# Kernel optimization log

Measured on AMD Instinct MI355X. Metric: run time of the kernel, lower is better.

## Reference

```python
import jax, jax.numpy as jnp
import numpy as np

VIEWS, N, D = 6, 20000, 512
BN_EPS = 1e-5


def setup_inputs() -> dict:
    key = jax.random.key(0)
    ks = jax.random.split(key, 8)
    s = 1.0 / np.sqrt(D)
    u = lambda k, shape: jax.random.uniform(k, shape, jnp.float32, -s, s)
    return {
        "latent_feature": jax.random.normal(ks[0], (VIEWS, N, D), jnp.float32),
        "WQ_w": u(ks[1], (D, D)), "WQ_b": u(ks[2], (D,)),
        "WK_w": u(ks[3], (D, D)), "WK_b": u(ks[4], (D,)),
        "WV_w": u(ks[5], (D, D)), "WV_b": u(ks[6], (D,)),
        "g_q": jnp.ones((D,), jnp.float32), "b_q": jnp.zeros((D,), jnp.float32),
        "g_k": jnp.ones((D,), jnp.float32), "b_k": jnp.zeros((D,), jnp.float32),
        "g_v": jnp.ones((D,), jnp.float32), "b_v": jnp.zeros((D,), jnp.float32),
    }


def _batchnorm(x, gamma, beta):
    # BatchNorm1d in training mode: stats over all (view, N) samples per channel
    mean = jnp.mean(x, axis=(0, 1), keepdims=True)
    var = jnp.mean((x - mean) ** 2, axis=(0, 1), keepdims=True)  # biased var
    return gamma * (x - mean) * jax.lax.rsqrt(var + BN_EPS) + beta


def _fro_normalize(x):
    # Frobenius norm per view over (N, D)
    n = jnp.sqrt(jnp.sum(x * x, axis=(1, 2), keepdims=True)) + 1e-8
    return x / n


def _multi_projection(P):
    dim = P.shape[0]
    P = 0.5 * (jax.nn.softmax(P, axis=0) + jax.nn.softmax(P, axis=1))
    for _ in range(10):  # fixed 10-step doubly-stochastic projection
        P1 = jnp.maximum(P, 0.0)
        P2 = P1 - (jnp.sum(P1, axis=1, keepdims=True) - 1.0) / dim
        P = P2 - (jnp.sum(P2, axis=0, keepdims=True) - 1.0) / dim
    return P


def reference(latent_feature, WQ_w, WQ_b, WK_w, WK_b, WV_w, WV_b,
              g_q, b_q, g_k, b_k, g_v, b_v):
    # latent_feature: [views, N, D]
    Q = _batchnorm(latent_feature @ WQ_w.T + WQ_b, g_q, b_q)
    K = _batchnorm(latent_feature @ WK_w.T + WK_b, g_k, b_k)
    V = _batchnorm(latent_feature @ WV_w.T + WV_b, g_v, b_v)
    Q, K, V = _fro_normalize(Q), _fro_normalize(K), _fro_normalize(V)
    P = jax.nn.sigmoid(jnp.einsum('ind,jnd->ij', Q, K))  # [views, views]
    P = _multi_projection(P)
    return jnp.einsum('ij,ind->jnd', P, V)  # [views, N, D]
```

## Files before the change

### kernel.cpp

```cpp
#include <hip/hip_runtime.h>

#define VIEWS 6
#define NPTS 20000
#define DIM 512
#define M_TOTAL (VIEWS * NPTS)

typedef __bf16 bf16_t;
typedef __attribute__((ext_vector_type(8))) __bf16 bf16x8;
typedef __attribute__((ext_vector_type(4))) float f32x4;

#define OFF_XB 0L
#define OFF_QB 122880000L
#define OFF_KB 245760000L
#define OFF_VB 368640000L
#define OFF_WB 491520000L
#define OFF_F32 493092864L
#define S_SUM 0
#define S_SSQ 9216
#define S_PPRE 18432
#define S_COEFA 18468
#define S_COEFC 20004
#define S_INVN 21540
#define S_P 21558
#define S_END 21594

__device__ __forceinline__ void gload_lds16(const void* gsrc, void* lds) {
    __builtin_amdgcn_global_load_lds(
        (const __attribute__((address_space(1))) unsigned int*)gsrc,
        (__attribute__((address_space(3))) unsigned int*)lds,
        16, 0, 0);
}

__global__ __launch_bounds__(256) void convert_bf16(
    const float* __restrict__ src, bf16_t* __restrict__ dst, long n8)
{
    long i = (long)blockIdx.x * blockDim.x + threadIdx.x;
    const long stride = (long)gridDim.x * blockDim.x;
    for (; i < n8; i += stride) {
        const float4* s = (const float4*)(src + i * 8);
        float4 x = s[0], y = s[1];
        bf16x8 o;
        o[0] = (bf16_t)x.x; o[1] = (bf16_t)x.y; o[2] = (bf16_t)x.z; o[3] = (bf16_t)x.w;
        o[4] = (bf16_t)y.x; o[5] = (bf16_t)y.y; o[6] = (bf16_t)y.z; o[7] = (bf16_t)y.w;
        *(bf16x8*)(dst + i * 8) = o;
    }
}

__global__ __launch_bounds__(256) void gemm_qkv_mfma(
    const bf16_t* __restrict__ XB, const bf16_t* __restrict__ WB,
    const float* __restrict__ b0, const float* __restrict__ b1,
    const float* __restrict__ b2,
    float* __restrict__ statS, float* __restrict__ statQ,
    bf16_t* __restrict__ QB, bf16_t* __restrict__ KB, bf16_t* __restrict__ VB)
{
    const int v  = blockIdx.z;
    const int n0 = blockIdx.x * 128;
    const int ct = blockIdx.y;
    const int t  = ct >> 2;
    const int c0 = (ct & 3) * 128;

    const int tid  = threadIdx.x;
    const int wid  = tid >> 6;
    const int lane = tid & 63;
    const int lr   = lane & 15;
    const int lk   = lane >> 4;
    const int wm   = wid >> 1;
    const int wn   = wid & 1;
    const int nvalid = min(128, NPTS - n0);

    __shared__ unsigned short As[128][64];
    __shared__ unsigned short Bs[128][64];
    __shared__ float redS[128];
    __shared__ float redQ[128];

    const bf16_t* Ag = XB + ((long)v * NPTS + n0) * DIM;
    const bf16_t* Bg = WB + ((long)t << 18) + ((long)c0 << 9);
    bf16_t* Obuf = (t == 0) ? QB : (t == 1) ? KB : VB;
    const float* bias = (t == 0) ? b0 : (t == 1) ? b1 : b2;

    f32x4 acc[4][4];
    const f32x4 zero4 = {0.f, 0.f, 0.f, 0.f};
#pragma unroll
    for (int i = 0; i < 4; ++i)
#pragma unroll
        for (int j = 0; j < 4; ++j) acc[i][j] = zero4;

    for (int k0 = 0; k0 < DIM; k0 += 64) {
        __syncthreads();
#pragma unroll
        for (int i = 0; i < 4; ++i) {
            const int base = i * 256 + wid * 64;
            const int myf  = base + lane;
            const int row  = myf >> 3;
            const int kc   = myf & 7;
            const int rowc = (row < nvalid) ? row : (nvalid - 1);
            gload_lds16(Ag + (long)rowc * DIM + k0 + kc * 8,
                        ((char*)&As[0][0]) + (long)base * 16);
            gload_lds16(Bg + (long)row * DIM + k0 + kc * 8,
                        ((char*)&Bs[0][0]) + (long)base * 16);
        }
        __syncthreads();
#pragma unroll
        for (int ks = 0; ks < 2; ++ks) {
            bf16x8 af[4], bfr[4];
#pragma unroll
            for (int f = 0; f < 4; ++f) {
                af[f]  = *(const bf16x8*)&As[wm * 64 + f * 16 + lr][ks * 32 + lk * 8];
                bfr[f] = *(const bf16x8*)&Bs[wn * 64 + f * 16 + lr][ks * 32 + lk * 8];
            }
#pragma unroll
            for (int fm = 0; fm < 4; ++fm)
#pragma unroll
                for (int fn = 0; fn < 4; ++fn)
                    acc[fm][fn] = __builtin_amdgcn_mfma_f32_16x16x32_bf16(
                        af[fm], bfr[fn], acc[fm][fn], 0, 0, 0);
        }
    }

    __syncthreads();
    if (tid < 128) { redS[tid] = 0.f; redQ[tid] = 0.f; }
    __syncthreads();

    float bcol[4];
#pragma unroll
    for (int fn = 0; fn < 4; ++fn) bcol[fn] = bias[c0 + wn * 64 + fn * 16 + lr];

#pragma unroll
    for (int fn = 0; fn < 4; ++fn) {
        float cs = 0.f, cq = 0.f;
        const int col = c0 + wn * 64 + fn * 16 + lr;
#pragma unroll
        for (int fm = 0; fm < 4; ++fm) {
            const int rbase = wm * 64 + fm * 16 + lk * 4;
#pragma unroll
            for (int r = 0; r < 4; ++r) {
                const int row = rbase + r;
                if (row < nvalid) {
                    float val = acc[fm][fn][r] + bcol[fn];
                    cs += val;
                    cq += val * val;
                    Obuf[((long)v * NPTS + n0 + row) * DIM + col] = (bf16_t)val;
                }
            }
        }
        atomicAdd(&redS[wn * 64 + fn * 16 + lr], cs);
        atomicAdd(&redQ[wn * 64 + fn * 16 + lr], cq);
    }
    __syncthreads();
    if (tid < 128) {
        atomicAdd(&statS[(((long)t * 6 + v) << 9) + c0 + tid], redS[tid]);
        atomicAdd(&statQ[(((long)t * 6 + v) << 9) + c0 + tid], redQ[tid]);
    }
}

__global__ __launch_bounds__(512) void finalize_stats(
    const float* __restrict__ gq, const float* __restrict__ beq,
    const float* __restrict__ gk, const float* __restrict__ bek,
    const float* __restrict__ gv, const float* __restrict__ bev,
    float* __restrict__ ws2)
{
    const int t = blockIdx.x;
    const int c = threadIdx.x;
    const float* g  = (t == 0) ? gq : (t == 1) ? gk : gv;
    const float* be = (t == 0) ? beq : (t == 1) ? bek : bev;
    const float* sumbuf = ws2 + S_SUM + (long)t * 6 * 512;
    const float* ssqbuf = ws2 + S_SSQ + (long)t * 6 * 512;

    float s[6], q[6];
    float tot = 0.f, totq = 0.f;
#pragma unroll
    for (int v = 0; v < 6; ++v) {
        s[v] = sumbuf[v * 512 + c];
        q[v] = ssqbuf[v * 512 + c];
        tot += s[v]; totq += q[v];
    }
    const float invM = 1.0f / (float)M_TOTAL;
    float mean = tot * invM;
    float var  = totq * invM - mean * mean;
    float a    = g[c] * rsqrtf(var + 1e-5f);
    float cc   = be[c] - a * mean;
    ws2[S_COEFA + t * 512 + c] = a;
    ws2[S_COEFC + t * 512 + c] = cc;

    __shared__ float red[512];
    for (int v = 0; v < 6; ++v) {
        red[c] = a * a * q[v] + 2.f * a * cc * s[v] + (float)NPTS * cc * cc;
        __syncthreads();
        for (int off = 256; off > 0; off >>= 1) {
            if (c < off) red[c] += red[c + off];
            __syncthreads();
        }
        if (c == 0) ws2[S_INVN + t * 6 + v] = 1.f / (sqrtf(red[0]) + 1e-8f);
        __syncthreads();
    }
}

__global__ __launch_bounds__(256) void qk_dot(
    const bf16_t* __restrict__ QB, const bf16_t* __restrict__ KB,
    float* __restrict__ ws2)
{
    float acc[36];
#pragma unroll
    for (int c = 0; c < 36; ++c) acc[c] = 0.f;

    const float* cA = ws2 + S_COEFA;
    const long total = (long)NPTS * 64;
    for (long it = (long)blockIdx.x * 256 + threadIdx.x; it < total;
         it += (long)gridDim.x * 256) {
        const int n  = (int)(it >> 6);
        const int d8 = (int)(it & 63);

        float w8[8];
#pragma unroll
        for (int e = 0; e < 8; ++e)
            w8[e] = cA[d8 * 8 + e] * cA[512 + d8 * 8 + e];

        float qw[6][8];
#pragma unroll
        for (int i = 0; i < 6; ++i) {
            bf16x8 qv = *(const bf16x8*)(QB + ((long)i * NPTS + n) * DIM + d8 * 8);
#pragma unroll
            for (int e = 0; e < 8; ++e) qw[i][e] = (float)qv[e] * w8[e];
        }
#pragma unroll
        for (int j = 0; j < 6; ++j) {
            bf16x8 kv = *(const bf16x8*)(KB + ((long)j * NPTS + n) * DIM + d8 * 8);
            float kf[8];
#pragma unroll
            for (int e = 0; e < 8; ++e) kf[e] = (float)kv[e];
#pragma unroll
            for (int i = 0; i < 6; ++i) {
                float d = 0.f;
#pragma unroll
                for (int e = 0; e < 8; ++e) d = fmaf(qw[i][e], kf[e], d);
                acc[i * 6 + j] += d;
            }
        }
    }

    __shared__ float part[36];
    if (threadIdx.x < 36) part[threadIdx.x] = 0.f;
    __syncthreads();
    const int lane = threadIdx.x & 63;
#pragma unroll
    for (int c = 0; c < 36; ++c) {
        float x = acc[c];
#pragma unroll
        for (int m = 1; m < 64; m <<= 1) x += __shfl_xor(x, m);
        if (lane == 0) atomicAdd(&part[c], x);
    }
    __syncthreads();
    if (threadIdx.x < 36) atomicAdd(&ws2[S_PPRE + threadIdx.x], part[threadIdx.x]);
}

__global__ __launch_bounds__(512) void project_kernel(float* __restrict__ ws2)
{
    const int c = threadIdx.x;
    __shared__ float red[512];
    const float aq = ws2[S_COEFA + c],       cq = ws2[S_COEFC + c];
    const float ak = ws2[S_COEFA + 512 + c], ck = ws2[S_COEFC + 512 + c];

    float vals[13];
#pragma unroll
    for (int i = 0; i < 6; ++i) vals[i]     = aq * ck * ws2[S_SUM + i * 512 + c];
#pragma unroll
    for (int j = 0; j < 6; ++j) vals[6 + j] = cq * ak * ws2[S_SUM + (6 + j) * 512 + c];
    vals[12] = cq * ck;

    float out13[13];
#pragma unroll
    for (int r = 0; r < 13; ++r) {
        red[c] = vals[r];
        __syncthreads();
        for (int off = 256; off > 0; off >>= 1) {
            if (c < off) red[c] += red[c + off];
            __syncthreads();
        }
        out13[r] = red[0];
        __syncthreads();
    }

    if (c != 0) return;

    const float* invn = ws2 + S_INVN;
    float p[6][6];
    for (int i = 0; i < 6; ++i)
        for (int j = 0; j < 6; ++j) {
            float raw = ws2[S_PPRE + i * 6 + j] + out13[i] + out13[6 + j] +
                        (float)NPTS * out13[12];
            float z = raw * invn[i] * invn[6 + j];
            p[i][j] = 1.f / (1.f + expf(-z));
        }
    float s0[6][6], s1[6][6];
    for (int j = 0; j < 6; ++j) {
        float m = -1e30f;
        for (int i = 0; i < 6; ++i) m = fmaxf(m, p[i][j]);
        float sum = 0.f;
        for (int i = 0; i < 6; ++i) { s0[i][j] = expf(p[i][j] - m); sum += s0[i][j]; }
        for (int i = 0; i < 6; ++i) s0[i][j] /= sum;
    }
    for (int i = 0; i < 6; ++i) {
        float m = -1e30f;
        for (int j = 0; j < 6; ++j) m = fmaxf(m, p[i][j]);
        float sum = 0.f;
        for (int j = 0; j < 6; ++j) { s1[i][j] = expf(p[i][j] - m); sum += s1[i][j]; }
        for (int j = 0; j < 6; ++j) s1[i][j] /= sum;
    }
    for (int i = 0; i < 6; ++i)
        for (int j = 0; j < 6; ++j) p[i][j] = 0.5f * (s0[i][j] + s1[i][j]);

    for (int itr = 0; itr < 10; ++itr) {
        float p1[6][6];
        for (int i = 0; i < 6; ++i)
            for (int j = 0; j < 6; ++j) p1[i][j] = fmaxf(p[i][j], 0.f);
        for (int i = 0; i < 6; ++i) {
            float rs = 0.f;
            for (int j = 0; j < 6; ++j) rs += p1[i][j];
            float adj = (rs - 1.f) * (1.f / 6.f);
            for (int j = 0; j < 6; ++j) p1[i][j] -= adj;
        }
        for (int j = 0; j < 6; ++j) {
            float cs = 0.f;
            for (int i = 0; i < 6; ++i) cs += p1[i][j];
            float adj = (cs - 1.f) * (1.f / 6.f);
            for (int i = 0; i < 6; ++i) p1[i][j] -= adj;
        }
        for (int i = 0; i < 6; ++i)
            for (int j = 0; j < 6; ++j) p[i][j] = p1[i][j];
    }
    for (int i = 0; i < 6; ++i)
        for (int j = 0; j < 6; ++j) ws2[S_P + i * 6 + j] = p[i][j];
}

__global__ __launch_bounds__(256) void combine_out(
    const bf16_t* __restrict__ VB, const float* __restrict__ ws2,
    float* __restrict__ out)
{
    float w[36];
#pragma unroll
    for (int c = 0; c < 36; ++c)
        w[c] = ws2[S_P + c] * ws2[S_INVN + 12 + c / 6];
    const float* av = ws2 + S_COEFA + 1024;
    const float* cv = ws2 + S_COEFC + 1024;

    const long total = (long)NPTS * 64;
    for (long it = (long)blockIdx.x * 256 + threadIdx.x; it < total;
         it += (long)gridDim.x * 256) {
        const int n  = (int)(it >> 6);
        const int d8 = (int)(it & 63);
        float a8[8], c8[8];
#pragma unroll
        for (int e = 0; e < 8; ++e) { a8[e] = av[d8 * 8 + e]; c8[e] = cv[d8 * 8 + e]; }

        float o[6][8];
#pragma unroll
        for (int j = 0; j < 6; ++j)
#pragma unroll
            for (int e = 0; e < 8; ++e) o[j][e] = 0.f;

#pragma unroll
        for (int i = 0; i < 6; ++i) {
            bf16x8 xv = *(const bf16x8*)(VB + ((long)i * NPTS + n) * DIM + d8 * 8);
            float vn[8];
#pragma unroll
            for (int e = 0; e < 8; ++e) vn[e] = fmaf(a8[e], (float)xv[e], c8[e]);
#pragma unroll
            for (int j = 0; j < 6; ++j) {
                const float wi = w[i * 6 + j];
#pragma unroll
                for (int e = 0; e < 8; ++e) o[j][e] = fmaf(wi, vn[e], o[j][e]);
            }
        }
#pragma unroll
        for (int j = 0; j < 6; ++j) {
            float* dst = out + ((long)j * NPTS + n) * DIM + d8 * 8;
            *(float4*)dst       = *(const float4*)&o[j][0];
            *(float4*)(dst + 4) = *(const float4*)&o[j][4];
        }
    }
}

extern "C" void kernel_launch(void* const* d_in, const int* in_sizes, int n_in,
                              void* d_out, int out_size, void* d_ws, size_t ws_size,
                              hipStream_t stream)
{
    const float* X   = (const float*)d_in[0];
    const float* Wq  = (const float*)d_in[1];
    const float* bq  = (const float*)d_in[2];
    const float* Wk  = (const float*)d_in[3];
    const float* bk  = (const float*)d_in[4];
    const float* Wv  = (const float*)d_in[5];
    const float* bv  = (const float*)d_in[6];
    const float* gq  = (const float*)d_in[7];
    const float* beq = (const float*)d_in[8];
    const float* gk  = (const float*)d_in[9];
    const float* bek = (const float*)d_in[10];
    const float* gv  = (const float*)d_in[11];
    const float* bev = (const float*)d_in[12];

    char* w = (char*)d_ws;
    bf16_t* XB = (bf16_t*)(w + OFF_XB);
    bf16_t* QB = (bf16_t*)(w + OFF_QB);
    bf16_t* KB = (bf16_t*)(w + OFF_KB);
    bf16_t* VB = (bf16_t*)(w + OFF_VB);
    bf16_t* WB = (bf16_t*)(w + OFF_WB);
    float* ws2 = (float*)(w + OFF_F32);
    float* out = (float*)d_out;

    hipMemsetAsync(ws2, 0, S_END * sizeof(float), stream);

    convert_bf16<<<2048, 256, 0, stream>>>(X, XB, (long)M_TOTAL * DIM / 8);
    convert_bf16<<<128, 256, 0, stream>>>(Wq, WB,           (long)DIM * DIM / 8);
    convert_bf16<<<128, 256, 0, stream>>>(Wk, WB + 262144,  (long)DIM * DIM / 8);
    convert_bf16<<<128, 256, 0, stream>>>(Wv, WB + 524288,  (long)DIM * DIM / 8);

    dim3 g1(157, 12, 6);
    gemm_qkv_mfma<<<g1, 256, 0, stream>>>(XB, WB, bq, bk, bv,
                                          ws2 + S_SUM, ws2 + S_SSQ, QB, KB, VB);
    finalize_stats<<<3, 512, 0, stream>>>(gq, beq, gk, bek, gv, bev, ws2);
    qk_dot<<<2048, 256, 0, stream>>>(QB, KB, ws2);
    project_kernel<<<1, 512, 0, stream>>>(ws2);
    combine_out<<<2048, 256, 0, stream>>>(VB, ws2, out);
}
```

Baseline: 1.110 ms.

## Fuse Q/K/V tiles sharing one A tile, swizzle LDS, remap blocks for XCD locality

Each GEMM block now loads one 64-row tile of X and computes 64 columns for all three of Q, K and V, so the A tile is reused three times instead of being loaded separately per projection. LDS rows use an XOR swizzle on the 16-byte chunk index to avoid bank conflicts. A 1D grid with an XCD-aware remap (orig&7 stride) places neighbouring tiles on the same chiplet for L2 reuse, and launch bounds request 4 blocks per CU. Tiles are smaller (64x64x3), which raises the number of blocks and adds per-block epilogue syncs for the three stat reductions.

After: 1.113 ms. About the same (+0.3%).

```diff
diff --git a/kernel.cpp b/kernel.cpp
--- a/kernel.cpp
+++ b/kernel.cpp
@@ -46,18 +46,21 @@
     }
 }
 
-__global__ __launch_bounds__(256) void gemm_qkv_mfma(
+__global__ __launch_bounds__(256, 4) void gemm_qkv_mfma(
     const bf16_t* __restrict__ XB, const bf16_t* __restrict__ WB,
     const float* __restrict__ b0, const float* __restrict__ b1,
     const float* __restrict__ b2,
     float* __restrict__ statS, float* __restrict__ statQ,
     bf16_t* __restrict__ QB, bf16_t* __restrict__ KB, bf16_t* __restrict__ VB)
 {
-    const int v  = blockIdx.z;
-    const int n0 = blockIdx.x * 128;
-    const int ct = blockIdx.y;
-    const int t  = ct >> 2;
-    const int c0 = (ct & 3) * 128;
+    const int orig = blockIdx.x;
+    const int L    = (orig & 7) * 1878 + (orig >> 3);
+    const int n0i  = L / 48;
+    const int rem  = L - n0i * 48;
+    const int v    = rem >> 3;
+    const int c0   = (rem & 7) << 6;
+    const int n0   = n0i * 64;
+    const int nvalid = min(64, NPTS - n0);
 
     const int tid  = threadIdx.x;
     const int wid  = tid >> 6;
@@ -66,90 +69,104 @@
     const int lk   = lane >> 4;
     const int wm   = wid >> 1;
     const int wn   = wid & 1;
-    const int nvalid = min(128, NPTS - n0);
-
-    __shared__ unsigned short As[128][64];
-    __shared__ unsigned short Bs[128][64];
-    __shared__ float redS[128];
-    __shared__ float redQ[128];
+
+    __shared__ char smem[32768];
 
     const bf16_t* Ag = XB + ((long)v * NPTS + n0) * DIM;
-    const bf16_t* Bg = WB + ((long)t << 18) + ((long)c0 << 9);
-    bf16_t* Obuf = (t == 0) ? QB : (t == 1) ? KB : VB;
-    const float* bias = (t == 0) ? b0 : (t == 1) ? b1 : b2;
-
-    f32x4 acc[4][4];
+
+    f32x4 acc[3][2][2];
     const f32x4 zero4 = {0.f, 0.f, 0.f, 0.f};
 #pragma unroll
-    for (int i = 0; i < 4; ++i)
-#pragma unroll
-        for (int j = 0; j < 4; ++j) acc[i][j] = zero4;
+    for (int t = 0; t < 3; ++t)
+#pragma unroll
+        for (int i = 0; i < 2; ++i)
+#pragma unroll
+            for (int j = 0; j < 2; ++j) acc[t][i][j] = zero4;
 
     for (int k0 = 0; k0 < DIM; k0 += 64) {
         __syncthreads();
 #pragma unroll
-        for (int i = 0; i < 4; ++i) {
+        for (int i = 0; i < 8; ++i) {
             const int base = i * 256 + wid * 64;
-            const int myf  = base + lane;
-            const int row  = myf >> 3;
-            const int kc   = myf & 7;
-            const int rowc = (row < nvalid) ? row : (nvalid - 1);
-            gload_lds16(Ag + (long)rowc * DIM + k0 + kc * 8,
-                        ((char*)&As[0][0]) + (long)base * 16);
-            gload_lds16(Bg + (long)row * DIM + k0 + kc * 8,
-                        ((char*)&Bs[0][0]) + (long)base * 16);
+            const int g    = base + lane;
+            const bf16_t* src;
+            if (g < 512) {
+                const int row = g >> 3;
+                const int kcs = (g & 7) ^ (row & 7);
+                const int rowc = (row < nvalid) ? row : (nvalid - 1);
+                src = Ag + (long)rowc * DIM + k0 + kcs * 8;
+            } else {
+                const int h   = g - 512;
+                const int t   = h >> 9;
+                const int idx = h & 511;
+                const int row = idx >> 3;
+                const int kcs = (idx & 7) ^ (row & 7);
+                src = WB + ((long)t << 18) + (long)(c0 + row) * DIM + k0 + kcs * 8;
+            }
+            gload_lds16(src, smem + (long)base * 16);
         }
         __syncthreads();
 #pragma unroll
         for (int ks = 0; ks < 2; ++ks) {
-            bf16x8 af[4], bfr[4];
-#pragma unroll
-            for (int f = 0; f < 4; ++f) {
-                af[f]  = *(const bf16x8*)&As[wm * 64 + f * 16 + lr][ks * 32 + lk * 8];
-                bfr[f] = *(const bf16x8*)&Bs[wn * 64 + f * 16 + lr][ks * 32 + lk * 8];
-            }
-#pragma unroll
-            for (int fm = 0; fm < 4; ++fm)
-#pragma unroll
-                for (int fn = 0; fn < 4; ++fn)
-                    acc[fm][fn] = __builtin_amdgcn_mfma_f32_16x16x32_bf16(
-                        af[fm], bfr[fn], acc[fm][fn], 0, 0, 0);
+            const int kc = ks * 4 + lk;
+            bf16x8 af[2];
+#pragma unroll
+            for (int fm = 0; fm < 2; ++fm) {
+                const int rowA = wm * 32 + fm * 16 + lr;
+                af[fm] = *(const bf16x8*)(smem + rowA * 128 + ((kc ^ (rowA & 7)) << 4));
+            }
+#pragma unroll
+            for (int t = 0; t < 3; ++t) {
+#pragma unroll
+                for (int fn = 0; fn < 2; ++fn) {
+                    const int rowB = wn * 32 + fn * 16 + lr;
+                    bf16x8 bf = *(const bf16x8*)(smem + 8192 + t * 8192 +
+                                                 rowB * 128 + ((kc ^ (rowB & 7)) << 4));
+#pragma unroll
+                    for (int fm = 0; fm < 2; ++fm)
+                        acc[t][fm][fn] = __builtin_amdgcn_mfma_f32_16x16x32_bf16(
+                            af[fm], bf, acc[t][fm][fn], 0, 0, 0);
+                }
+            }
         }
     }
 
     __syncthreads();
-    if (tid < 128) { redS[tid] = 0.f; redQ[tid] = 0.f; }
-    __syncthreads();
-
-    float bcol[4];
-#pragma unroll
-    for (int fn = 0; fn < 4; ++fn) bcol[fn] = bias[c0 + wn * 64 + fn * 16 + lr];
-
-#pragma unroll
-    for (int fn = 0; fn < 4; ++fn) {
-        float cs = 0.f, cq = 0.f;
-        const int col = c0 + wn * 64 + fn * 16 + lr;
-#pragma unroll
-        for (int fm = 0; fm < 4; ++fm) {
-            const int rbase = wm * 64 + fm * 16 + lk * 4;
-#pragma unroll
-            for (int r = 0; r < 4; ++r) {
-                const int row = rbase + r;
-                if (row < nvalid) {
-                    float val = acc[fm][fn][r] + bcol[fn];
-                    cs += val;
-                    cq += val * val;
-                    Obuf[((long)v * NPTS + n0 + row) * DIM + col] = (bf16_t)val;
+    float* redS = (float*)smem;
+    float* redQ = redS + 64;
+    for (int t = 0; t < 3; ++t) {
+        if (tid < 128) redS[tid] = 0.f;
+        __syncthreads();
+        bf16_t* Obuf = (t == 0) ? QB : (t == 1) ? KB : VB;
+        const float* bias = (t == 0) ? b0 : (t == 1) ? b1 : b2;
+#pragma unroll
+        for (int fn = 0; fn < 2; ++fn) {
+            const int cl  = wn * 32 + fn * 16 + lr;
+            const int col = c0 + cl;
+            const float bv_ = bias[col];
+            float cs = 0.f, cq = 0.f;
+#pragma unroll
+            for (int fm = 0; fm < 2; ++fm) {
+#pragma unroll
+                for (int r = 0; r < 4; ++r) {
+                    const int row = wm * 32 + fm * 16 + lk * 4 + r;
+                    if (row < nvalid) {
+                        float val = acc[t][fm][fn][r] + bv_;
+                        cs += val;
+                        cq += val * val;
+                        Obuf[((long)v * NPTS + n0 + row) * DIM + col] = (bf16_t)val;
+                    }
                 }
             }
-        }
-        atomicAdd(&redS[wn * 64 + fn * 16 + lr], cs);
-        atomicAdd(&redQ[wn * 64 + fn * 16 + lr], cq);
-    }
-    __syncthreads();
-    if (tid < 128) {
-        atomicAdd(&statS[(((long)t * 6 + v) << 9) + c0 + tid], redS[tid]);
-        atomicAdd(&statQ[(((long)t * 6 + v) << 9) + c0 + tid], redQ[tid]);
+            atomicAdd(&redS[cl], cs);
+            atomicAdd(&redQ[cl], cq);
+        }
+        __syncthreads();
+        if (tid < 64) {
+            atomicAdd(&statS[(((long)t * 6 + v) << 9) + c0 + tid], redS[tid]);
+            atomicAdd(&statQ[(((long)t * 6 + v) << 9) + c0 + tid], redQ[tid]);
+        }
+        __syncthreads();
     }
 }
 
@@ -414,9 +431,8 @@
     convert_bf16<<<128, 256, 0, stream>>>(Wk, WB + 262144,  (long)DIM * DIM / 8);
     convert_bf16<<<128, 256, 0, stream>>>(Wv, WB + 524288,  (long)DIM * DIM / 8);
 
-    dim3 g1(157, 12, 6);
-    gemm_qkv_mfma<<<g1, 256, 0, stream>>>(XB, WB, bq, bk, bv,
-                                          ws2 + S_SUM, ws2 + S_SSQ, QB, KB, VB);
+    gemm_qkv_mfma<<<15024, 256, 0, stream>>>(XB, WB, bq, bk, bv,
+                                             ws2 + S_SUM, ws2 + S_SSQ, QB, KB, VB);
     finalize_stats<<<3, 512, 0, stream>>>(gq, beq, gk, bek, gv, bev, ws2);
     qk_dot<<<2048, 256, 0, stream>>>(QB, KB, ws2);
     project_kernel<<<1, 512, 0, stream>>>(ws2);
```
